# Kernel tuning notes

Hardware: AMD Instinct MI355X
Metric: run time of the kernel (lower is better)

The kernel has to match this reference:

```python
import jax, jax.numpy as jnp
import numpy as np

N_EMBD = 384
N_HEAD = 6
BLOCK_SIZE = 256


def setup_inputs() -> dict:
    key = jax.random.key(0)
    ks = jax.random.split(key, 5)
    B, T = 128, 256
    x = jax.random.normal(ks[0], (B, T, N_EMBD), dtype=jnp.float32)
    # torch nn.Linear weights are (out_features, in_features)
    w_attn = jax.random.normal(ks[1], (3 * N_EMBD, N_EMBD), dtype=jnp.float32) * (1.0 / np.sqrt(N_EMBD))
    b_attn = jax.random.normal(ks[2], (3 * N_EMBD,), dtype=jnp.float32) * 0.02
    w_proj = jax.random.normal(ks[3], (N_EMBD, N_EMBD), dtype=jnp.float32) * (1.0 / np.sqrt(N_EMBD))
    b_proj = jax.random.normal(ks[4], (N_EMBD,), dtype=jnp.float32) * 0.02
    return {"x": x, "w_attn": w_attn, "b_attn": b_attn, "w_proj": w_proj, "b_proj": b_proj}


def reference(x, w_attn, b_attn, w_proj, b_proj):
    B, T, C = x.shape
    hd = C // N_HEAD  # head dim = 64
    qkv = x @ w_attn.T + b_attn                      # [B,T,3C]
    q, k, v = jnp.split(qkv, 3, axis=2)
    # [B,T,C] -> [B,H,T,hd]
    q = q.reshape(B, T, N_HEAD, hd).transpose(0, 2, 1, 3)
    k = k.reshape(B, T, N_HEAD, hd).transpose(0, 2, 1, 3)
    v = v.reshape(B, T, N_HEAD, hd).transpose(0, 2, 1, 3)
    att = jnp.einsum("bhqd,bhkd->bhqk", q, k) * (1.0 / np.sqrt(hd))
    causal = jnp.tril(jnp.ones((T, T), dtype=bool))
    att = jnp.where(causal, att, -jnp.inf)
    att = jax.nn.softmax(att, axis=-1)
    y = jnp.einsum("bhqk,bhkd->bhqd", att, v)        # [B,H,T,hd]
    y = y.transpose(0, 2, 1, 3).reshape(B, T, C)
    return y @ w_proj.T + b_proj
```

## Files before the change

### kernel.cpp

```cpp
#include <hip/hip_runtime.h>
#include <stdint.h>


typedef unsigned short u16;
typedef __attribute__((ext_vector_type(8))) short short8;
typedef __attribute__((ext_vector_type(4))) short short4v;
typedef __attribute__((ext_vector_type(4))) float float4v;

__device__ __forceinline__ u16 f2b(float f){
  union { float f; uint32_t u; } cv; cv.f = f;
  uint32_t u = cv.u;
  u += 0x7FFFu + ((u >> 16) & 1u);
  return (u16)(u >> 16);
}

__device__ __forceinline__ float4v mfma16(short8 a, short8 b, float4v c){
  return __builtin_amdgcn_mfma_f32_16x16x32_bf16(a, b, c, 0, 0, 0);
}

__device__ __forceinline__ void gld16(const void* g, void* l){
  __builtin_amdgcn_global_load_lds((__attribute__((address_space(1))) const void*)g,
                                   (__attribute__((address_space(3))) void*)l, 16, 0, 0);
}

__global__ __launch_bounds__(256) void cvt3(
    const float* __restrict__ a, u16* __restrict__ da, int na,
    const float* __restrict__ b, u16* __restrict__ db, int nb,
    const float* __restrict__ c, u16* __restrict__ dc, int nc)
{
  const int total = na + nb + nc;
  for (int i = blockIdx.x * blockDim.x + threadIdx.x; i < total;
       i += gridDim.x * blockDim.x){
    const float* s; u16* d; int j = i;
    if (j < na)           { s = a; d = da; }
    else if (j < na + nb) { j -= na; s = b; d = db; }
    else                  { j -= na + nb; s = c; d = dc; }
    const float4 v = ((const float4*)s)[j];
    ushort4 o;
    o.x = f2b(v.x); o.y = f2b(v.y); o.z = f2b(v.z); o.w = f2b(v.w);
    ((ushort4*)d)[j] = o;
  }
}

template<int BM, int EPI>
__global__ __launch_bounds__(256, 2) void gemm_k(
    const u16* __restrict__ A, const u16* __restrict__ B,
    const float* __restrict__ bias, void* __restrict__ Cout,
    u16* __restrict__ Vt, const int M, const int N, const int K, const int CS)
{
  constexpr int NN    = (BM == 256) ? 8 : 4;
  constexpr int AB    = BM * 32;
  constexpr int ACH   = BM / 64;
  constexpr int BOFF  = 3 * AB;
  constexpr int SHSZ  = 3 * AB + 3 * 4096;
  __shared__ __align__(16) u16 SH[SHSZ];

  const int tid  = threadIdx.x;
  const int lane = tid & 63;
  const int wave = tid >> 6;
  const int lrow = lane & 15;
  const int g    = lane >> 4;

  const int NYT   = N >> 7;
  const int xpx   = (M / BM) >> 3;
  const int id    = blockIdx.x;
  const int local = id >> 3;
  const int xtl   = local / NYT;
  const int yt    = local - xtl * NYT;
  const int tm = ((id & 7) * xpx + xtl) * BM;
  const int tn = yt * 128;
  const int wm = (BM == 256) ? wave * 64 : (wave >> 1) * 64;
  const int wn = (BM == 256) ? 0          : (wave & 1) * 64;

  float4v acc[4][NN];
  #pragma unroll
  for (int i = 0; i < 4; ++i)
    #pragma unroll
    for (int j = 0; j < NN; ++j) acc[i][j] = (float4v){0.f, 0.f, 0.f, 0.f};

  const int srow = lane >> 2;
  const int sg   = ((lane & 3) ^ ((lane >> 3) & 3)) << 3;
  const int key  = (lrow >> 1) & 3;

  auto STAGE = [&](int kt, int buf){
    #pragma unroll
    for (int j = 0; j < ACH; ++j){
      const int c = wave * ACH + j;
      const int row = c * 16 + srow;
      gld16(A + (size_t)(tm + row) * K + kt * 32 + sg, &SH[buf * AB + c * 512]);
    }
    #pragma unroll
    for (int j = 0; j < 2; ++j){
      const int c = wave * 2 + j;
      const int row = c * 16 + srow;
      gld16(B + (size_t)(tn + row) * K + kt * 32 + sg, &SH[BOFF + buf * 4096 + c * 512]);
    }
  };

  const int nkt = K >> 5;
  STAGE(0, 0);
  STAGE(1, 1);
  int b0 = 0;
  for (int kt = 0; kt < nkt; ++kt){
    if (kt + 1 < nkt){
      if (BM == 256) asm volatile("s_waitcnt vmcnt(6)" ::: "memory");
      else           asm volatile("s_waitcnt vmcnt(4)" ::: "memory");
    } else {
      asm volatile("s_waitcnt vmcnt(0)" ::: "memory");
    }
    __builtin_amdgcn_s_barrier();

    const u16* Ac = &SH[b0 * AB];
    const u16* Bc = &SH[BOFF + b0 * 4096];
    short8 af[4], bf[NN];
    #pragma unroll
    for (int i = 0; i < 4; ++i)
      af[i] = *(const short8*)&Ac[(wm + i * 16 + lrow) * 32 + ((g ^ key) << 3)];
    #pragma unroll
    for (int ni = 0; ni < NN; ++ni)
      bf[ni] = *(const short8*)&Bc[(wn + ni * 16 + lrow) * 32 + ((g ^ key) << 3)];

    asm volatile("s_waitcnt lgkmcnt(0)" ::: "memory");
    __builtin_amdgcn_sched_barrier(0);
    __builtin_amdgcn_s_barrier();

    const int bs = (b0 == 0) ? 2 : b0 - 1;
    if (kt + 2 < nkt) STAGE(kt + 2, bs);

    __builtin_amdgcn_s_setprio(1);
    #pragma unroll
    for (int ni = 0; ni < NN; ++ni)
      #pragma unroll
      for (int mi = 0; mi < 4; ++mi)
        acc[mi][ni] = mfma16(af[mi], bf[ni], acc[mi][ni]);
    __builtin_amdgcn_s_setprio(0);

    b0 = (b0 == 2) ? 0 : b0 + 1;
  }

  if (EPI == 1 && tn >= 768){
    const int bb = tm >> 8;
    #pragma unroll
    for (int ni = 0; ni < NN; ++ni){
      const int vcol0 = tn - 768 + ni * 16;
      const int hh = vcol0 >> 6;
      const int dd = (vcol0 & 63) + lrow;
      const float bs = bias[tn + ni * 16 + lrow];
      u16* vbase = Vt + ((size_t)(bb * 6 + hh) * 64 + dd) * 256;
      #pragma unroll
      for (int mi = 0; mi < 4; ++mi){
        #pragma unroll
        for (int r = 0; r < 4; ++r){
          const int t = wm + mi * 16 + g * 4 + r;
          vbase[t] = f2b(acc[mi][ni][r] + bs);
        }
      }
    }
  } else if (EPI == 1){
    u16* wreg = &SH[wave * 8704];
    #pragma unroll
    for (int mi = 0; mi < 4; ++mi)
      #pragma unroll
      for (int ni = 0; ni < NN; ++ni){
        const float bs = bias[tn + ni * 16 + lrow];
        #pragma unroll
        for (int r = 0; r < 4; ++r)
          wreg[(mi * 16 + g * 4 + r) * 136 + ni * 16 + lrow] =
              f2b(acc[mi][ni][r] + bs);
      }
    asm volatile("s_waitcnt lgkmcnt(0)" ::: "memory");
    #pragma unroll
    for (int i = 0; i < 16; ++i){
      const int row = i * 4 + (lane >> 4);
      const short8 v = *(const short8*)&wreg[row * 136 + (lane & 15) * 8];
      *(short8*)((u16*)Cout + (size_t)(tm + wm + row) * CS + tn + (lane & 15) * 8) = v;
    }
  } else {
    float* wregf = (float*)&SH[0] + wave * 2304;
    #pragma unroll
    for (int half = 0; half < 2; ++half){
      #pragma unroll
      for (int mi = 0; mi < 4; ++mi)
        #pragma unroll
        for (int nj = 0; nj < 2; ++nj){
          const int ni = half * 2 + nj;
          const float bs = bias[tn + wn + ni * 16 + lrow];
          #pragma unroll
          for (int r = 0; r < 4; ++r)
            wregf[(mi * 16 + g * 4 + r) * 36 + nj * 16 + lrow] =
                acc[mi][ni][r] + bs;
        }
      asm volatile("s_waitcnt lgkmcnt(0)" ::: "memory");
      #pragma unroll
      for (int i = 0; i < 8; ++i){
        const int row = i * 8 + (lane >> 3);
        const float4 v = *(const float4*)&wregf[row * 36 + (lane & 7) * 4];
        *(float4*)((float*)Cout + (size_t)(tm + wm + row) * CS
                   + tn + wn + half * 32 + (lane & 7) * 4) = v;
      }
      asm volatile("s_waitcnt lgkmcnt(0)" ::: "memory");
    }
  }
}

__global__ __launch_bounds__(256) void attn_k(
    const u16* __restrict__ qkv, const u16* __restrict__ vt,
    u16* __restrict__ y)
{
  __shared__ u16 Klds[256 * 64];
  __shared__ u16 Vlds[64 * 256];
  const int tid  = threadIdx.x;
  const int lane = tid & 63;
  const int wave = tid >> 6;
  const int lrow = lane & 15;
  const int g    = lane >> 4;
  const int bh = blockIdx.x;
  const int b = bh / 6, h = bh % 6;
  const u16* qb  = qkv + (size_t)b * 256 * 768 + h * 64;
  const u16* kb  = qb + 384;
  const u16* vtb = vt + (size_t)(b * 6 + h) * 64 * 256;

  #pragma unroll
  for (int j = 0; j < 8; ++j){
    const int c = wave * 8 + j;
    const int row = c * 8 + (lane >> 3);
    const int col = (((lane & 7) ^ (lane >> 3)) << 3);
    gld16(kb + (size_t)row * 768 + col, &Klds[c * 512]);
  }
  #pragma unroll
  for (int j = 0; j < 8; ++j){
    const int c  = wave * 8 + j;
    const int dd = c * 2 + (lane >> 5);
    const int q  = lane & 31;
    gld16(vtb + (size_t)dd * 256 + ((q ^ (dd & 7)) << 3), &Vlds[c * 512]);
  }
  __syncthreads();

  #pragma unroll
  for (int it = 0; it < 4; ++it){
    const int rb = (it == 0) ? wave : (it == 1) ? 15 - wave
                 : (it == 2) ? wave + 4 : 11 - wave;
    const int q0 = rb * 16;
    const u16* qrow = qb + (size_t)(q0 + lrow) * 768 + g * 8;
    const short8 qf0 = *(const short8*)(qrow);
    const short8 qf1 = *(const short8*)(qrow + 32);

    float4v s[16];
    #pragma unroll
    for (int nt = 0; nt < 16; ++nt){
      if (nt <= rb){
        const int row = nt * 16 + lrow;
        const int swk = lrow & 7;
        const short8 k0 = *(const short8*)&Klds[row * 64 + ((g ^ swk) << 3)];
        const short8 k1 = *(const short8*)&Klds[row * 64 + (((4 + g) ^ swk) << 3)];
        float4v a = (float4v){0.f, 0.f, 0.f, 0.f};
        a = mfma16(k0, qf0, a);
        a = mfma16(k1, qf1, a);
        if (nt == rb){
          #pragma unroll
          for (int r = 0; r < 4; ++r)
            a[r] = (g * 4 + r > lrow) ? -1e30f : a[r];
        }
        s[nt] = a;
      }
    }

    float mx = -1e30f;
    #pragma unroll
    for (int nt = 0; nt < 16; ++nt) if (nt <= rb){
      #pragma unroll
      for (int r = 0; r < 4; ++r) mx = fmaxf(mx, s[nt][r]);
    }
    mx = fmaxf(mx, __shfl_xor(mx, 16));
    mx = fmaxf(mx, __shfl_xor(mx, 32));
    float sum = 0.f;
    #pragma unroll
    for (int nt = 0; nt < 16; ++nt) if (nt <= rb){
      #pragma unroll
      for (int r = 0; r < 4; ++r){
        const float p = exp2f((s[nt][r] - mx) * 0.18033688011112042f);
        s[nt][r] = p;
        sum += p;
      }
    }
    sum += __shfl_xor(sum, 16);
    sum += __shfl_xor(sum, 32);
    const float rs = 1.f / sum;
    #pragma unroll
    for (int nt = 0; nt < 16; ++nt) if (nt <= rb) s[nt] *= rs;

    float4v o0 = (float4v){0,0,0,0}, o1 = (float4v){0,0,0,0};
    float4v o2 = (float4v){0,0,0,0}, o3 = (float4v){0,0,0,0};
    const int swk = lrow & 7;
    #pragma unroll
    for (int kt = 0; kt < 8; ++kt){
      if (2 * kt <= rb){
        short8 pa;
        #pragma unroll
        for (int r = 0; r < 4; ++r) pa[r] = (short)f2b(s[2 * kt][r]);
        if (2 * kt + 1 <= rb){
          #pragma unroll
          for (int r = 0; r < 4; ++r) pa[4 + r] = (short)f2b(s[2 * kt + 1][r]);
        } else {
          #pragma unroll
          for (int r = 0; r < 4; ++r) pa[4 + r] = 0;
        }
        const int plo_e = (((kt * 4 +     (g >> 1)) ^ swk) << 3) + ((g & 1) << 2);
        const int phi_e = (((kt * 4 + 2 + (g >> 1)) ^ swk) << 3) + ((g & 1) << 2);
        #pragma unroll
        for (int dt = 0; dt < 4; ++dt){
          const u16* vrow = &Vlds[(size_t)(dt * 16 + lrow) * 256];
          const short4v vlo = *(const short4v*)&vrow[plo_e];
          const short4v vhi = *(const short4v*)&vrow[phi_e];
          const short8 bf = __builtin_shufflevector(vlo, vhi, 0,1,2,3,4,5,6,7);
          if      (dt == 0) o0 = mfma16(pa, bf, o0);
          else if (dt == 1) o1 = mfma16(pa, bf, o1);
          else if (dt == 2) o2 = mfma16(pa, bf, o2);
          else              o3 = mfma16(pa, bf, o3);
        }
      }
    }

    u16* yb = y + (size_t)(b * 256 + q0) * 384 + h * 64;
    #pragma unroll
    for (int r = 0; r < 4; ++r){
      const int q = g * 4 + r;
      yb[(size_t)q * 384 +  0 + lrow] = f2b(o0[r]);
      yb[(size_t)q * 384 + 16 + lrow] = f2b(o1[r]);
      yb[(size_t)q * 384 + 32 + lrow] = f2b(o2[r]);
      yb[(size_t)q * 384 + 48 + lrow] = f2b(o3[r]);
    }
  }
}

extern "C" void kernel_launch(void* const* d_in, const int* in_sizes, int n_in,
                              void* d_out, int out_size, void* d_ws, size_t ws_size,
                              hipStream_t stream)
{
  const float* x      = (const float*)d_in[0];
  const float* w_attn = (const float*)d_in[1];
  const float* b_attn = (const float*)d_in[2];
  const float* w_proj = (const float*)d_in[3];
  const float* b_proj = (const float*)d_in[4];
  float* out = (float*)d_out;

  char* ws = (char*)d_ws;
  u16* xb  = (u16*)(ws);
  u16* wab = (u16*)(ws + 25165824);
  u16* wpb = (u16*)(ws + 26050560);
  u16* qkv = (u16*)(ws + 26345472);
  u16* vt  = (u16*)(ws + 76677120);
  u16* yb  = (u16*)(ws + 101842944);
  if (ws_size < 127008768) return;

  cvt3<<<2048, 256, 0, stream>>>(x, xb, 3145728,
                                 w_attn, wab, 110592,
                                 w_proj, wpb, 36864);
  gemm_k<256,1><<<1152, 256, 0, stream>>>(xb, wab, b_attn, qkv, vt, 32768, 1152, 384, 768);
  attn_k<<<768, 256, 0, stream>>>(qkv, vt, yb);
  gemm_k<128,0><<<768, 256, 0, stream>>>(yb, wpb, b_proj, out, nullptr, 32768, 384, 384, 384);
}
```

Measured before the change: 122.6 us.

## Store GEMM epilogues directly to global and defer softmax normalization to output

The GEMM epilogues no longer stage accumulators through LDS for coalesced stores. They now write each element directly to global memory, and the V-transpose path now includes the per-wave column offset. In attention, the 1/sum scaling moves from every probability onto the final output rows via lane shuffles, and probabilities are converted to bf16 by truncation instead of rounding. Together these cut per-element ALU and LDS work, but scalar uncoalesced global stores and truncation rounding error are added in exchange.

```diff
diff --git a/kernel.cpp b/kernel.cpp
--- a/kernel.cpp
+++ b/kernel.cpp
@@ -12,6 +12,11 @@
   uint32_t u = cv.u;
   u += 0x7FFFu + ((u >> 16) & 1u);
   return (u16)(u >> 16);
+}
+
+__device__ __forceinline__ u16 f2b_t(float f){
+  union { float f; uint32_t u; } cv; cv.f = f;
+  return (u16)(cv.u >> 16);
 }
 
 __device__ __forceinline__ float4v mfma16(short8 a, short8 b, float4v c){
@@ -142,10 +147,10 @@
     const int bb = tm >> 8;
     #pragma unroll
     for (int ni = 0; ni < NN; ++ni){
-      const int vcol0 = tn - 768 + ni * 16;
+      const int vcol0 = tn + wn - 768 + ni * 16;
       const int hh = vcol0 >> 6;
       const int dd = (vcol0 & 63) + lrow;
-      const float bs = bias[tn + ni * 16 + lrow];
+      const float bs = bias[tn + wn + ni * 16 + lrow];
       u16* vbase = Vt + ((size_t)(bb * 6 + hh) * 64 + dd) * 256;
       #pragma unroll
       for (int mi = 0; mi < 4; ++mi){
@@ -156,49 +161,21 @@
         }
       }
     }
-  } else if (EPI == 1){
-    u16* wreg = &SH[wave * 8704];
-    #pragma unroll
-    for (int mi = 0; mi < 4; ++mi)
+  } else {
+    #pragma unroll
+    for (int mi = 0; mi < 4; ++mi){
       #pragma unroll
       for (int ni = 0; ni < NN; ++ni){
-        const float bs = bias[tn + ni * 16 + lrow];
+        const int gcol = tn + wn + ni * 16 + lrow;
+        const float bs = bias[gcol];
         #pragma unroll
-        for (int r = 0; r < 4; ++r)
-          wreg[(mi * 16 + g * 4 + r) * 136 + ni * 16 + lrow] =
-              f2b(acc[mi][ni][r] + bs);
-      }
-    asm volatile("s_waitcnt lgkmcnt(0)" ::: "memory");
-    #pragma unroll
-    for (int i = 0; i < 16; ++i){
-      const int row = i * 4 + (lane >> 4);
-      const short8 v = *(const short8*)&wreg[row * 136 + (lane & 15) * 8];
-      *(short8*)((u16*)Cout + (size_t)(tm + wm + row) * CS + tn + (lane & 15) * 8) = v;
-    }
-  } else {
-    float* wregf = (float*)&SH[0] + wave * 2304;
-    #pragma unroll
-    for (int half = 0; half < 2; ++half){
-      #pragma unroll
-      for (int mi = 0; mi < 4; ++mi)
-        #pragma unroll
-        for (int nj = 0; nj < 2; ++nj){
-          const int ni = half * 2 + nj;
-          const float bs = bias[tn + wn + ni * 16 + lrow];
-          #pragma unroll
-          for (int r = 0; r < 4; ++r)
-            wregf[(mi * 16 + g * 4 + r) * 36 + nj * 16 + lrow] =
-                acc[mi][ni][r] + bs;
-        }
-      asm volatile("s_waitcnt lgkmcnt(0)" ::: "memory");
-      #pragma unroll
-      for (int i = 0; i < 8; ++i){
-        const int row = i * 8 + (lane >> 3);
-        const float4 v = *(const float4*)&wregf[row * 36 + (lane & 7) * 4];
-        *(float4*)((float*)Cout + (size_t)(tm + wm + row) * CS
-                   + tn + wn + half * 32 + (lane & 7) * 4) = v;
-      }
-      asm volatile("s_waitcnt lgkmcnt(0)" ::: "memory");
+        for (int r = 0; r < 4; ++r){
+          const int grow = tm + wm + mi * 16 + g * 4 + r;
+          const float v = acc[mi][ni][r] + bs;
+          if (EPI == 1) ((u16*)Cout)[(size_t)grow * CS + gcol] = f2b(v);
+          else          ((float*)Cout)[(size_t)grow * CS + gcol] = v;
+        }
+      }
     }
   }
 }
@@ -286,8 +263,9 @@
     sum += __shfl_xor(sum, 16);
     sum += __shfl_xor(sum, 32);
     const float rs = 1.f / sum;
-    #pragma unroll
-    for (int nt = 0; nt < 16; ++nt) if (nt <= rb) s[nt] *= rs;
+    float rsq[4];
+    #pragma unroll
+    for (int r = 0; r < 4; ++r) rsq[r] = __shfl(rs, g * 4 + r);
 
     float4v o0 = (float4v){0,0,0,0}, o1 = (float4v){0,0,0,0};
     float4v o2 = (float4v){0,0,0,0}, o3 = (float4v){0,0,0,0};
@@ -297,10 +275,10 @@
       if (2 * kt <= rb){
         short8 pa;
         #pragma unroll
-        for (int r = 0; r < 4; ++r) pa[r] = (short)f2b(s[2 * kt][r]);
+        for (int r = 0; r < 4; ++r) pa[r] = (short)f2b_t(s[2 * kt][r]);
         if (2 * kt + 1 <= rb){
           #pragma unroll
-          for (int r = 0; r < 4; ++r) pa[4 + r] = (short)f2b(s[2 * kt + 1][r]);
+          for (int r = 0; r < 4; ++r) pa[4 + r] = (short)f2b_t(s[2 * kt + 1][r]);
         } else {
           #pragma unroll
           for (int r = 0; r < 4; ++r) pa[4 + r] = 0;
@@ -325,10 +303,10 @@
     #pragma unroll
     for (int r = 0; r < 4; ++r){
       const int q = g * 4 + r;
-      yb[(size_t)q * 384 +  0 + lrow] = f2b(o0[r]);
-      yb[(size_t)q * 384 + 16 + lrow] = f2b(o1[r]);
-      yb[(size_t)q * 384 + 32 + lrow] = f2b(o2[r]);
-      yb[(size_t)q * 384 + 48 + lrow] = f2b(o3[r]);
+      yb[(size_t)q * 384 +  0 + lrow] = f2b(o0[r] * rsq[r]);
+      yb[(size_t)q * 384 + 16 + lrow] = f2b(o1[r] * rsq[r]);
+      yb[(size_t)q * 384 + 32 + lrow] = f2b(o2[r] * rsq[r]);
+      yb[(size_t)q * 384 + 48 + lrow] = f2b(o3[r] * rsq[r]);
     }
   }
 }
```

After: 117.3 us. 1.04x faster.
